# Kernel optimization log

Hardware: AMD Instinct MI355X
Metric: run time of the kernel (lower is better)

## Reference

```python
import jax, jax.numpy as jnp
import numpy as np

HEADS = 16
DIM_HEAD = 64
LN_EPS = 1e-3  # keras LayerNormalization default


def setup_inputs() -> dict:
    key = jax.random.key(0)
    ks = jax.random.split(key, 4)
    B, N, D = 8, 512, 1024
    inner = HEADS * DIM_HEAD  # 1024
    return {
        "x": jax.random.normal(ks[0], (B, N, D), dtype=jnp.float32),
        "w_qkv": jax.random.normal(ks[1], (D, 3 * inner), dtype=jnp.float32) * (D ** -0.5),
        "reattn_w": jax.random.normal(ks[2], (HEADS, HEADS), dtype=jnp.float32),
        "ln_gamma": jnp.ones((HEADS,), dtype=jnp.float32),
        "ln_beta": jnp.zeros((HEADS,), dtype=jnp.float32),
        "w_out": jax.random.normal(ks[3], (inner, D), dtype=jnp.float32) * (inner ** -0.5),
        "b_out": jnp.zeros((D,), dtype=jnp.float32),
    }


def reference(x, w_qkv, reattn_w, ln_gamma, ln_beta, w_out, b_out):
    B, N, D = x.shape
    H, dh = HEADS, DIM_HEAD
    scale = dh ** -0.5

    qkv = x @ w_qkv  # [B, N, 3*H*dh]
    q, k, v = jnp.split(qkv, 3, axis=-1)
    # b n (h d) -> b h n d
    to_heads = lambda t: t.reshape(B, N, H, dh).transpose(0, 2, 1, 3)
    q, k, v = to_heads(q), to_heads(k), to_heads(v)

    dots = jnp.einsum("bhid,bhjd->bhij", q, k) * scale  # [B, H, N, N]
    attn = jax.nn.softmax(dots, axis=-1)

    # re-attention: mix across heads
    attn = jnp.einsum("bhij,hg->bgij", attn, reattn_w)

    # LayerNorm over the head axis (axis=1), keras default eps
    mean = jnp.mean(attn, axis=1, keepdims=True)
    var = jnp.var(attn, axis=1, keepdims=True)
    attn = (attn - mean) * jax.lax.rsqrt(var + LN_EPS)
    attn = attn * ln_gamma[None, :, None, None] + ln_beta[None, :, None, None]

    out = jnp.einsum("bhij,bhjd->bhid", attn, v)  # [B, H, N, dh]
    out = out.transpose(0, 2, 1, 3).reshape(B, N, H * dh)  # b h n d -> b n (h d)
    return out @ w_out + b_out
```

## Files before the change

kernel.cpp:

```cpp
#include <hip/hip_runtime.h>
#include <math.h>

#define BB 8
#define NN 512
#define DD 1024
#define HH 16
#define DH 64
#define INNER 1024
#define QKV3 3072
#define PSTR (NN * NN + 64)

typedef __attribute__((ext_vector_type(8))) short short8;
typedef __attribute__((ext_vector_type(4))) float f32x4;

#define AS1 __attribute__((address_space(1)))
#define AS3 __attribute__((address_space(3)))

__device__ __forceinline__ float4 ld4(const float* p) { return *(const float4*)p; }

__device__ __forceinline__ unsigned short f2bf(float f) {
    unsigned u = __float_as_uint(f);
    return (unsigned short)((u + 0x7fffu + ((u >> 16) & 1u)) >> 16);
}
__device__ __forceinline__ float bf2f(unsigned short u) {
    return __uint_as_float(((unsigned)u) << 16);
}

__global__ void preprocess(const float* __restrict__ x, unsigned short* __restrict__ xb,
                           const float* __restrict__ wq, unsigned short* __restrict__ wqT,
                           const float* __restrict__ wo, unsigned short* __restrict__ woT) {
    __shared__ float t[32][33];
    const int tid = threadIdx.x;
    const int bx = blockIdx.x;
    if (bx < 4096) {
        size_t i = ((size_t)bx * 256 + tid) * 4;
        float4 v = ld4(x + i);
        ushort4 o;
        o.x = f2bf(v.x); o.y = f2bf(v.y); o.z = f2bf(v.z); o.w = f2bf(v.w);
        *(ushort4*)(xb + i) = o;
        return;
    }
    const float* in; unsigned short* out; int K, N, n0, k0;
    if (bx < 7168) {
        const int bb = bx - 4096;
        in = wq; out = wqT; K = DD; N = QKV3;
        n0 = (bb % 96) * 32; k0 = (bb / 96) * 32;
    } else {
        const int bb = bx - 7168;
        in = wo; out = woT; K = INNER; N = INNER;
        n0 = (bb & 31) * 32; k0 = (bb >> 5) * 32;
    }
    const int tx = tid & 31, ty = tid >> 5;
#pragma unroll
    for (int l = 0; l < 4; ++l)
        t[ty + 8 * l][tx] = in[(size_t)(k0 + ty + 8 * l) * N + n0 + tx];
    __syncthreads();
#pragma unroll
    for (int l = 0; l < 4; ++l)
        out[(size_t)(n0 + ty + 8 * l) * K + k0 + tx] = f2bf(t[tx][ty + 8 * l]);
}

__device__ __forceinline__ void stage128(const unsigned short* __restrict__ A,
                                         const unsigned short* __restrict__ Bt,
                                         int K, int bm, int bn, int kt,
                                         short* sb, int w, int l) {
#pragma unroll
    for (int t = 0; t < 2; ++t) {
        const int q = w * 2 + t;
        const int li = q * 512 + l * 8;
        const int row = li >> 5, kc = li & 31;
        __builtin_amdgcn_global_load_lds(
            (const AS1 void*)(A + (size_t)(bm + row) * K + kt * 32 + kc),
            (AS3 void*)(sb + q * 512), 16, 0, 0);
        __builtin_amdgcn_global_load_lds(
            (const AS1 void*)(Bt + (size_t)(bn + row) * K + kt * 32 + kc),
            (AS3 void*)(sb + 4096 + q * 512), 16, 0, 0);
    }
}

__global__ __launch_bounds__(256) void gemm_bf16(
    const unsigned short* __restrict__ A, const unsigned short* __restrict__ Bt,
    float* __restrict__ C, const float* __restrict__ bias, int M, int N, int K) {
    __shared__ __align__(16) short lds_[2 * 8192];
    const int tid = threadIdx.x;
    const int w = tid >> 6, l = tid & 63;
    const int bm = blockIdx.y * 128, bn = blockIdx.x * 128;
    const int wm = (w >> 1) * 64, wn = (w & 1) * 64;
    const int lrow = l & 15, lq = l >> 4;
    const int NT = K >> 5;

    f32x4 acc[4][4];
#pragma unroll
    for (int i = 0; i < 4; ++i)
#pragma unroll
        for (int j = 0; j < 4; ++j) acc[i][j] = (f32x4){0.f, 0.f, 0.f, 0.f};

    stage128(A, Bt, K, bm, bn, 0, lds_, w, l);
    asm volatile("s_waitcnt vmcnt(0)" ::: "memory");
    __builtin_amdgcn_s_barrier();

    for (int t = 0; t < NT; ++t) {
        const int s = t & 1;
        if (t + 1 < NT)
            stage128(A, Bt, K, bm, bn, t + 1, lds_ + (s ^ 1) * 8192, w, l);
        const short* As_ = lds_ + s * 8192;
        const short* Bs_ = As_ + 4096;
        short8 a[4], b[4];
#pragma unroll
        for (int i = 0; i < 4; ++i)
            a[i] = *(const short8*)(As_ + (wm + i * 16 + lrow) * 32 + lq * 8);
#pragma unroll
        for (int j = 0; j < 4; ++j)
            b[j] = *(const short8*)(Bs_ + (wn + j * 16 + lrow) * 32 + lq * 8);

        asm volatile("s_waitcnt lgkmcnt(0)" ::: "memory");
        __builtin_amdgcn_sched_barrier(0);

        __builtin_amdgcn_s_setprio(1);
#pragma unroll
        for (int i = 0; i < 4; ++i)
#pragma unroll
            for (int j = 0; j < 4; ++j)
                acc[i][j] = __builtin_amdgcn_mfma_f32_16x16x32_bf16(a[i], b[j], acc[i][j], 0, 0, 0);
        __builtin_amdgcn_s_setprio(0);

        asm volatile("s_waitcnt vmcnt(0)" ::: "memory");
        __builtin_amdgcn_s_barrier();
    }

#pragma unroll
    for (int i = 0; i < 4; ++i)
#pragma unroll
        for (int j = 0; j < 4; ++j) {
            const int col = bn + wn + j * 16 + lrow;
            const float bv = bias ? bias[col] : 0.f;
#pragma unroll
            for (int r = 0; r < 4; ++r) {
                const int row = bm + wm + i * 16 + lq * 4 + r;
                C[(size_t)row * N + col] = acc[i][j][r] + bv;
            }
        }
}

__device__ __forceinline__ void stage_st(const unsigned short* __restrict__ G, int K,
                                         int row0, int kt, short* dst_half,
                                         int w, int l) {
    const int grow = row0 + w * 16 + (l >> 2);
    const int gcol = kt * 32 + (((l & 3) * 8) ^ ((l & 32) ? 16 : 0));
    __builtin_amdgcn_global_load_lds(
        (const AS1 void*)(G + (size_t)grow * K + gcol),
        (AS3 void*)(dst_half + w * 512), 16, 0, 0);
}

__global__ __launch_bounds__(512, 4) void gemm256_bf(
    const unsigned short* __restrict__ A, const unsigned short* __restrict__ Bt,
    unsigned short* __restrict__ C, int M, int N, int K) {
    __shared__ __align__(16) short lds_[2 * 12288];
    const int tid = threadIdx.x;
    const int w = tid >> 6, l = tid & 63;
    const int wmi = w >> 1, wni = w & 1;
    const int lrow = l & 15, lq = l >> 4;
    const int bm = blockIdx.y * 256, bn = blockIdx.x * 128;
    const int NT = K >> 5;

    const int aoff = lrow * 32 + ((lq * 8) ^ ((lrow & 8) ? 16 : 0));

    f32x4 acc[4][4];
#pragma unroll
    for (int i = 0; i < 4; ++i)
#pragma unroll
        for (int j = 0; j < 4; ++j) acc[i][j] = (f32x4){0.f, 0.f, 0.f, 0.f};

    stage_st(A,  K, bm,       0, lds_ + 0,    w, l);
    stage_st(A,  K, bm + 128, 0, lds_ + 4096, w, l);
    stage_st(Bt, K, bn,       0, lds_ + 8192, w, l);
    asm volatile("s_waitcnt vmcnt(0)" ::: "memory");
    __builtin_amdgcn_s_barrier();

    for (int t = 0; t < NT; ++t) {
        const int s = t & 1;
        if (t + 1 < NT) {
            short* nb = lds_ + (s ^ 1) * 12288;
            stage_st(A,  K, bm,       t + 1, nb,        w, l);
            stage_st(A,  K, bm + 128, t + 1, nb + 4096, w, l);
            stage_st(Bt, K, bn,       t + 1, nb + 8192, w, l);
        }
        const short* cb = lds_ + s * 12288;
        short8 a[4], b[4];
#pragma unroll
        for (int i = 0; i < 4; ++i)
            a[i] = *(const short8*)(cb + (wmi * 4 + i) * 512 + aoff);
#pragma unroll
        for (int j = 0; j < 4; ++j)
            b[j] = *(const short8*)(cb + 8192 + (wni * 4 + j) * 512 + aoff);

        asm volatile("s_waitcnt lgkmcnt(0)" ::: "memory");
        __builtin_amdgcn_sched_barrier(0);

        __builtin_amdgcn_s_setprio(1);
#pragma unroll
        for (int i = 0; i < 4; ++i)
#pragma unroll
            for (int j = 0; j < 4; ++j)
                acc[i][j] = __builtin_amdgcn_mfma_f32_16x16x32_bf16(a[i], b[j], acc[i][j], 0, 0, 0);
        __builtin_amdgcn_s_setprio(0);

        asm volatile("s_waitcnt vmcnt(0)" ::: "memory");
        __builtin_amdgcn_s_barrier();
    }

#pragma unroll
    for (int i = 0; i < 4; ++i)
#pragma unroll
        for (int j = 0; j < 4; ++j) {
            const int col = bn + wni * 64 + j * 16 + lrow;
#pragma unroll
            for (int r = 0; r < 4; ++r) {
                const int row = bm + wmi * 64 + i * 16 + lq * 4 + r;
                C[(size_t)row * N + col] = f2bf(acc[i][j][r]);
            }
        }
}

__global__ __launch_bounds__(256) void scores_tv(
    const unsigned short* __restrict__ qkvb, unsigned short* __restrict__ attnb,
    unsigned short* __restrict__ vT, float* __restrict__ lsum2) {
    __shared__ unsigned short sh[256 * 64 + 4 * 16 * 68];
    const int bx = blockIdx.x;
    const int tid = threadIdx.x;

    if (bx >= 2048) {
        const int t = bx - 2048;
        const int j0 = (t & 15) * 32;
        const int d0 = ((t >> 4) & 1) * 32;
        const int bh = t >> 5;
        const int h = bh & 15, b = bh >> 4;
        unsigned short (*tt)[33] = (unsigned short(*)[33])sh;
        const int tx = tid & 31, ty = tid >> 5;
        const unsigned short* src = qkvb + (size_t)(b * NN) * QKV3 + 2 * INNER + h * DH;
#pragma unroll
        for (int k = 0; k < 4; ++k)
            tt[ty + 8 * k][tx] = src[(size_t)(j0 + ty + 8 * k) * QKV3 + d0 + tx];
        __syncthreads();
        unsigned short* dst = vT + (size_t)bh * DH * NN;
#pragma unroll
        for (int k = 0; k < 4; ++k)
            dst[(size_t)(d0 + ty + 8 * k) * NN + j0 + tx] = tt[tx][ty + 8 * k];
        return;
    }

    unsigned short* Ks = sh;
    unsigned short* obuf = sh + 16384;
    const int bh = bx & 127;
    const int h = bh & 15, b = bh >> 4;
    const int jh = (bx >> 7) & 1;
    const int w = tid >> 6, l = tid & 63;
    const int i0 = (bx >> 8) * 64 + w * 16;
    const int lrow = l & 15, lq = l >> 4;

    const unsigned short* kbase =
        qkvb + (size_t)(b * NN + jh * 256) * QKV3 + INNER + h * DH;
#pragma unroll
    for (int i = 0; i < 8; ++i) {
        const int r = (w * 8 + i) * 8 + (l >> 3);
        const int c = (l & 7) ^ (r & 7);
        __builtin_amdgcn_global_load_lds(
            (const AS1 void*)(kbase + (size_t)r * QKV3 + c * 8),
            (AS3 void*)(Ks + (w * 8 + i) * 512), 16, 0, 0);
    }

    const unsigned short* qb = qkvb + (size_t)(b * NN) * QKV3 + h * DH + lq * 8;
    const short8 qf0 = *(const short8*)(qb + (size_t)(i0 + lrow) * QKV3);
    const short8 qf1 = *(const short8*)(qb + (size_t)(i0 + lrow) * QKV3 + 32);

    asm volatile("s_waitcnt vmcnt(0)" ::: "memory");
    __syncthreads();

    unsigned short* obase = attnb + (size_t)bh * PSTR + (size_t)i0 * NN + jh * 256;
    unsigned short* ob = obuf + (w * 16) * 68;
    const int sw = lrow & 7;
    float lacc = 0.f;
#pragma unroll
    for (int jt = 0; jt < 16; ++jt) {
        const int R = jt * 16 + lrow;
        const short8 kf0 = *(const short8*)(Ks + R * 64 + ((lq ^ sw) * 8));
        const short8 kf1 = *(const short8*)(Ks + R * 64 + (((4 + lq) ^ sw) * 8));
        f32x4 acc = (f32x4){0.f, 0.f, 0.f, 0.f};
        acc = __builtin_amdgcn_mfma_f32_16x16x32_bf16(kf0, qf0, acc, 0, 0, 0);
        acc = __builtin_amdgcn_mfma_f32_16x16x32_bf16(kf1, qf1, acc, 0, 0, 0);
        float e0 = __expf(acc[0] * 0.125f);
        float e1 = __expf(acc[1] * 0.125f);
        float e2 = __expf(acc[2] * 0.125f);
        float e3 = __expf(acc[3] * 0.125f);
        lacc += (e0 + e1) + (e2 + e3);
        ushort4 o;
        o.x = f2bf(e0); o.y = f2bf(e1); o.z = f2bf(e2); o.w = f2bf(e3);
        *(ushort4*)(ob + lrow * 68 + (jt & 3) * 16 + lq * 4) = o;
        if ((jt & 3) == 3) {
            const int jb = (jt >> 2) * 64;
#pragma unroll
            for (int q = 0; q < 4; ++q) {
                const int rr = q * 4 + (l >> 4);
                const int cc = l & 15;
                *(ushort4*)(obase + (size_t)rr * NN + jb + cc * 4) =
                    *(const ushort4*)(ob + rr * 68 + cc * 4);
            }
        }
    }
    lacc += __shfl_xor(lacc, 16, 64);
    lacc += __shfl_xor(lacc, 32, 64);
    if (lq == 0)
        lsum2[(size_t)jh * BB * HH * NN + (size_t)bh * NN + i0 + lrow] = lacc;
}

__global__ void reattn_ln_bf(unsigned short* __restrict__ attnb,
                             const float* __restrict__ lsum2,
                             const float* __restrict__ rw,
                             const float* __restrict__ gamma,
                             const float* __restrict__ beta) {
    __shared__ float w[16][16];
    __shared__ float gs[16], bs[16];
    const int tid = threadIdx.x;
    ((float*)w)[tid] = rw[tid];
    if (tid < 16) { gs[tid] = gamma[tid]; bs[tid] = beta[tid]; }
    __syncthreads();

    const size_t idx = (size_t)blockIdx.x * 256 + tid;
    const int j4 = (int)(idx & 127);
    const int i = (int)((idx >> 7) & 511);
    const int b = (int)(idx >> 16);
    unsigned short* base = attnb + (size_t)(b * HH) * PSTR + (size_t)i * NN + j4 * 4;
    const float* l0 = lsum2 + (size_t)(b * HH) * NN + i;
    const float* l1 = l0 + (size_t)BB * HH * NN;

    float v[16][4];
#pragma unroll
    for (int h = 0; h < 16; ++h) {
        const float linv = 1.0f / (l0[h * NN] + l1[h * NN]);
        ushort4 u = *(const ushort4*)(base + (size_t)h * PSTR);
        v[h][0] = bf2f(u.x) * linv; v[h][1] = bf2f(u.y) * linv;
        v[h][2] = bf2f(u.z) * linv; v[h][3] = bf2f(u.w) * linv;
    }
    float o[16][4];
    float me[4] = {0.f, 0.f, 0.f, 0.f};
#pragma unroll
    for (int g = 0; g < 16; ++g) {
        float s0 = 0.f, s1 = 0.f, s2 = 0.f, s3 = 0.f;
#pragma unroll
        for (int h = 0; h < 16; ++h) {
            const float wg = w[h][g];
            s0 += v[h][0] * wg; s1 += v[h][1] * wg;
            s2 += v[h][2] * wg; s3 += v[h][3] * wg;
        }
        o[g][0] = s0; o[g][1] = s1; o[g][2] = s2; o[g][3] = s3;
        me[0] += s0; me[1] += s1; me[2] += s2; me[3] += s3;
    }
#pragma unroll
    for (int r = 0; r < 4; ++r) me[r] *= 0.0625f;
    float va[4] = {0.f, 0.f, 0.f, 0.f};
#pragma unroll
    for (int g = 0; g < 16; ++g)
#pragma unroll
        for (int r = 0; r < 4; ++r) {
            float d = o[g][r] - me[r];
            va[r] += d * d;
        }
    float ri[4];
#pragma unroll
    for (int r = 0; r < 4; ++r) ri[r] = rsqrtf(va[r] * 0.0625f + 1e-3f);
#pragma unroll
    for (int g = 0; g < 16; ++g) {
        ushort4 u;
        u.x = f2bf((o[g][0] - me[0]) * ri[0] * gs[g] + bs[g]);
        u.y = f2bf((o[g][1] - me[1]) * ri[1] * gs[g] + bs[g]);
        u.z = f2bf((o[g][2] - me[2]) * ri[2] * gs[g] + bs[g]);
        u.w = f2bf((o[g][3] - me[3]) * ri[3] * gs[g] + bs[g]);
        *(ushort4*)(base + (size_t)g * PSTR) = u;
    }
}

__device__ __forceinline__ void stage_pv(const unsigned short* __restrict__ pb,
                                         const unsigned short* __restrict__ vb,
                                         int j0, short* Ps, short* Vs,
                                         int w, int l, int lr8, int swd) {
#pragma unroll
    for (int t = 0; t < 4; ++t) {
        int c = w * 4 + t;
        int r = c * 8 + lr8;
        __builtin_amdgcn_global_load_lds(
            (const AS1 void*)(pb + (size_t)r * NN + j0 + swd),
            (AS3 void*)(Ps + c * 512), 16, 0, 0);
    }
#pragma unroll
    for (int t = 0; t < 2; ++t) {
        int c = w * 2 + t;
        int d = c * 8 + lr8;
        __builtin_amdgcn_global_load_lds(
            (const AS1 void*)(vb + (size_t)d * NN + j0 + swd),
            (AS3 void*)(Vs + c * 512), 16, 0, 0);
    }
}

__global__ __launch_bounds__(256) void pv_mfma(
    const unsigned short* __restrict__ attnb, const unsigned short* __restrict__ vT,
    unsigned short* __restrict__ outhb) {
    const int bh = blockIdx.x;
    const int h = bh & 15, b = bh >> 4;
    const int i0 = blockIdx.y * 128;
    __shared__ __align__(16) short Ps[2][128 * 64];
    __shared__ __align__(16) short Vs[2][64 * 64];
    const int tid = threadIdx.x;
    const int w = tid >> 6, l = tid & 63;
    const int lrow = l & 15, lq = l >> 4;
    const int lr8 = l >> 3;
    const int swd = ((l & 7) ^ (lr8 & 7)) * 8;

    f32x4 acc[2][4];
#pragma unroll
    for (int ic = 0; ic < 2; ++ic)
#pragma unroll
        for (int dt = 0; dt < 4; ++dt) acc[ic][dt] = (f32x4){0.f, 0.f, 0.f, 0.f};

    const unsigned short* pb = attnb + (size_t)bh * PSTR + (size_t)i0 * NN;
    const unsigned short* vb = vT + (size_t)bh * DH * NN;

    stage_pv(pb, vb, 0, Ps[0], Vs[0], w, l, lr8, swd);
    asm volatile("s_waitcnt vmcnt(0)" ::: "memory");
    __builtin_amdgcn_s_barrier();

    for (int js = 0; js < 8; ++js) {
        const int s = js & 1;
        if (js + 1 < 8)
            stage_pv(pb, vb, (js + 1) * 64, Ps[s ^ 1], Vs[s ^ 1], w, l, lr8, swd);

        short8 vf[8], pf[4];
#pragma unroll
        for (int kh = 0; kh < 2; ++kh) {
#pragma unroll
            for (int dt = 0; dt < 4; ++dt)
                vf[kh * 4 + dt] = *(const short8*)(
                    &Vs[s][(dt * 16 + lrow) * 64 + (((kh * 4 + lq) ^ (lrow & 7)) * 8)]);
#pragma unroll
            for (int ic = 0; ic < 2; ++ic)
                pf[kh * 2 + ic] = *(const short8*)(
                    &Ps[s][(w * 32 + ic * 16 + lrow) * 64 + (((kh * 4 + lq) ^ (lrow & 7)) * 8)]);
        }

        asm volatile("s_waitcnt lgkmcnt(0)" ::: "memory");
        __builtin_amdgcn_sched_barrier(0);

        __builtin_amdgcn_s_setprio(1);
#pragma unroll
        for (int kh = 0; kh < 2; ++kh)
#pragma unroll
            for (int ic = 0; ic < 2; ++ic)
#pragma unroll
                for (int dt = 0; dt < 4; ++dt)
                    acc[ic][dt] = __builtin_amdgcn_mfma_f32_16x16x32_bf16(
                        vf[kh * 4 + dt], pf[kh * 2 + ic], acc[ic][dt], 0, 0, 0);
        __builtin_amdgcn_s_setprio(0);

        asm volatile("s_waitcnt vmcnt(0)" ::: "memory");
        __builtin_amdgcn_s_barrier();
    }

#pragma unroll
    for (int ic = 0; ic < 2; ++ic) {
        unsigned short* orow = outhb +
            ((size_t)(b * NN + i0 + w * 32 + ic * 16 + lrow)) * INNER + h * DH + lq * 4;
#pragma unroll
        for (int dt = 0; dt < 4; ++dt) {
            ushort4 o;
            o.x = f2bf(acc[ic][dt][0]); o.y = f2bf(acc[ic][dt][1]);
            o.z = f2bf(acc[ic][dt][2]); o.w = f2bf(acc[ic][dt][3]);
            *(ushort4*)(orow + dt * 16) = o;
        }
    }
}

extern "C" void kernel_launch(void* const* d_in, const int* in_sizes, int n_in,
                              void* d_out, int out_size, void* d_ws, size_t ws_size,
                              hipStream_t stream) {
    const float* x        = (const float*)d_in[0];
    const float* w_qkv    = (const float*)d_in[1];
    const float* reattn_w = (const float*)d_in[2];
    const float* ln_gamma = (const float*)d_in[3];
    const float* ln_beta  = (const float*)d_in[4];
    const float* w_out    = (const float*)d_in[5];
    const float* b_out    = (const float*)d_in[6];
    float* out = (float*)d_out;

    unsigned short* qkvb  = (unsigned short*)d_ws;
    unsigned short* attnb = qkvb + (size_t)BB * NN * QKV3;
    unsigned short* vTb   = attnb + (size_t)BB * HH * PSTR;
    unsigned short* outhb = vTb + (size_t)BB * HH * DH * NN;
    unsigned short* xb    = outhb + (size_t)BB * NN * INNER;
    unsigned short* wqkvT = xb + (size_t)BB * NN * DD;
    unsigned short* woutT = wqkvT + (size_t)DD * QKV3;
    float*          lsum2 = (float*)(woutT + (size_t)INNER * INNER);

    dim3 blk(256);

    preprocess<<<dim3(8192), blk, 0, stream>>>(x, xb, w_qkv, wqkvT, w_out, woutT);

    gemm256_bf<<<dim3(QKV3 / 128, (BB * NN) / 256), dim3(512), 0, stream>>>(
        xb, wqkvT, qkvb, BB * NN, QKV3, DD);

    scores_tv<<<dim3(6144), blk, 0, stream>>>(qkvb, attnb, vTb, lsum2);

    reattn_ln_bf<<<dim3((BB * NN * NN) / 1024), blk, 0, stream>>>(
        attnb, lsum2, reattn_w, ln_gamma, ln_beta);

    pv_mfma<<<dim3(BB * HH, NN / 128), blk, 0, stream>>>(attnb, vTb, outhb);

    gemm_bf16<<<dim3(INNER / 128, (BB * NN) / 128), blk, 0, stream>>>(
        outhb, woutT, out, b_out, BB * NN, INNER, INNER);
}
```

Baseline: 201.9 us.

## Fuse re-attention LayerNorm into the PV matmul kernel

```diff
diff --git a/kernel.cpp b/kernel.cpp
--- a/kernel.cpp
+++ b/kernel.cpp
@@ -313,166 +313,129 @@
         lsum2[(size_t)jh * BB * HH * NN + (size_t)bh * NN + i0 + lrow] = lacc;
 }
 
-__global__ void reattn_ln_bf(unsigned short* __restrict__ attnb,
-                             const float* __restrict__ lsum2,
-                             const float* __restrict__ rw,
-                             const float* __restrict__ gamma,
-                             const float* __restrict__ beta) {
-    __shared__ float w[16][16];
-    __shared__ float gs[16], bs[16];
-    const int tid = threadIdx.x;
-    ((float*)w)[tid] = rw[tid];
-    if (tid < 16) { gs[tid] = gamma[tid]; bs[tid] = beta[tid]; }
-    __syncthreads();
-
-    const size_t idx = (size_t)blockIdx.x * 256 + tid;
-    const int j4 = (int)(idx & 127);
-    const int i = (int)((idx >> 7) & 511);
-    const int b = (int)(idx >> 16);
-    unsigned short* base = attnb + (size_t)(b * HH) * PSTR + (size_t)i * NN + j4 * 4;
-    const float* l0 = lsum2 + (size_t)(b * HH) * NN + i;
-    const float* l1 = l0 + (size_t)BB * HH * NN;
-
-    float v[16][4];
-#pragma unroll
-    for (int h = 0; h < 16; ++h) {
-        const float linv = 1.0f / (l0[h * NN] + l1[h * NN]);
-        ushort4 u = *(const ushort4*)(base + (size_t)h * PSTR);
-        v[h][0] = bf2f(u.x) * linv; v[h][1] = bf2f(u.y) * linv;
-        v[h][2] = bf2f(u.z) * linv; v[h][3] = bf2f(u.w) * linv;
-    }
-    float o[16][4];
-    float me[4] = {0.f, 0.f, 0.f, 0.f};
-#pragma unroll
-    for (int g = 0; g < 16; ++g) {
-        float s0 = 0.f, s1 = 0.f, s2 = 0.f, s3 = 0.f;
-#pragma unroll
-        for (int h = 0; h < 16; ++h) {
-            const float wg = w[h][g];
-            s0 += v[h][0] * wg; s1 += v[h][1] * wg;
-            s2 += v[h][2] * wg; s3 += v[h][3] * wg;
-        }
-        o[g][0] = s0; o[g][1] = s1; o[g][2] = s2; o[g][3] = s3;
-        me[0] += s0; me[1] += s1; me[2] += s2; me[3] += s3;
-    }
-#pragma unroll
-    for (int r = 0; r < 4; ++r) me[r] *= 0.0625f;
-    float va[4] = {0.f, 0.f, 0.f, 0.f};
-#pragma unroll
-    for (int g = 0; g < 16; ++g)
-#pragma unroll
-        for (int r = 0; r < 4; ++r) {
-            float d = o[g][r] - me[r];
-            va[r] += d * d;
-        }
-    float ri[4];
-#pragma unroll
-    for (int r = 0; r < 4; ++r) ri[r] = rsqrtf(va[r] * 0.0625f + 1e-3f);
-#pragma unroll
-    for (int g = 0; g < 16; ++g) {
-        ushort4 u;
-        u.x = f2bf((o[g][0] - me[0]) * ri[0] * gs[g] + bs[g]);
-        u.y = f2bf((o[g][1] - me[1]) * ri[1] * gs[g] + bs[g]);
-        u.z = f2bf((o[g][2] - me[2]) * ri[2] * gs[g] + bs[g]);
-        u.w = f2bf((o[g][3] - me[3]) * ri[3] * gs[g] + bs[g]);
-        *(ushort4*)(base + (size_t)g * PSTR) = u;
-    }
-}
-
-__device__ __forceinline__ void stage_pv(const unsigned short* __restrict__ pb,
-                                         const unsigned short* __restrict__ vb,
-                                         int j0, short* Ps, short* Vs,
-                                         int w, int l, int lr8, int swd) {
-#pragma unroll
-    for (int t = 0; t < 4; ++t) {
-        int c = w * 4 + t;
-        int r = c * 8 + lr8;
-        __builtin_amdgcn_global_load_lds(
-            (const AS1 void*)(pb + (size_t)r * NN + j0 + swd),
-            (AS3 void*)(Ps + c * 512), 16, 0, 0);
-    }
-#pragma unroll
-    for (int t = 0; t < 2; ++t) {
-        int c = w * 2 + t;
-        int d = c * 8 + lr8;
-        __builtin_amdgcn_global_load_lds(
-            (const AS1 void*)(vb + (size_t)d * NN + j0 + swd),
-            (AS3 void*)(Vs + c * 512), 16, 0, 0);
-    }
-}
-
-__global__ __launch_bounds__(256) void pv_mfma(
+__global__ __launch_bounds__(512) void reattn_pv(
     const unsigned short* __restrict__ attnb, const unsigned short* __restrict__ vT,
+    const float* __restrict__ lsum2, const float* __restrict__ rw,
+    const float* __restrict__ gamma, const float* __restrict__ beta,
     unsigned short* __restrict__ outhb) {
-    const int bh = blockIdx.x;
-    const int h = bh & 15, b = bh >> 4;
-    const int i0 = blockIdx.y * 128;
-    __shared__ __align__(16) short Ps[2][128 * 64];
-    __shared__ __align__(16) short Vs[2][64 * 64];
+    __shared__ unsigned short Ash[16 * 16 * 64];
+    __shared__ float wsh[16][16];
+    __shared__ float linv[16][16];
+    __shared__ float gsh[16], bsh[16];
+
+    const int b = blockIdx.x >> 5;
+    const int i0 = (blockIdx.x & 31) * 16;
     const int tid = threadIdx.x;
     const int w = tid >> 6, l = tid & 63;
     const int lrow = l & 15, lq = l >> 4;
-    const int lr8 = l >> 3;
-    const int swd = ((l & 7) ^ (lr8 & 7)) * 8;
+
+    if (tid < 256) {
+        ((float*)wsh)[tid] = rw[tid];
+        const int h = tid >> 4, i = tid & 15;
+        const float s =
+            lsum2[(size_t)(b * HH + h) * NN + i0 + i] +
+            lsum2[(size_t)BB * HH * NN + (size_t)(b * HH + h) * NN + i0 + i];
+        linv[h][i] = 1.0f / s;
+    }
+    if (tid < 16) { gsh[tid] = gamma[tid]; bsh[tid] = beta[tid]; }
+
+    const int ri = w * 2 + (l >> 5);
+    const int rj = (l & 31) * 2;
+    const unsigned short* ebase =
+        attnb + (size_t)(b * HH) * PSTR + (size_t)(i0 + ri) * NN + rj;
 
     f32x4 acc[2][4];
 #pragma unroll
-    for (int ic = 0; ic < 2; ++ic)
-#pragma unroll
-        for (int dt = 0; dt < 4; ++dt) acc[ic][dt] = (f32x4){0.f, 0.f, 0.f, 0.f};
-
-    const unsigned short* pb = attnb + (size_t)bh * PSTR + (size_t)i0 * NN;
-    const unsigned short* vb = vT + (size_t)bh * DH * NN;
-
-    stage_pv(pb, vb, 0, Ps[0], Vs[0], w, l, lr8, swd);
-    asm volatile("s_waitcnt vmcnt(0)" ::: "memory");
-    __builtin_amdgcn_s_barrier();
-
-    for (int js = 0; js < 8; ++js) {
-        const int s = js & 1;
-        if (js + 1 < 8)
-            stage_pv(pb, vb, (js + 1) * 64, Ps[s ^ 1], Vs[s ^ 1], w, l, lr8, swd);
-
-        short8 vf[8], pf[4];
-#pragma unroll
-        for (int kh = 0; kh < 2; ++kh) {
-#pragma unroll
-            for (int dt = 0; dt < 4; ++dt)
-                vf[kh * 4 + dt] = *(const short8*)(
-                    &Vs[s][(dt * 16 + lrow) * 64 + (((kh * 4 + lq) ^ (lrow & 7)) * 8)]);
-#pragma unroll
-            for (int ic = 0; ic < 2; ++ic)
-                pf[kh * 2 + ic] = *(const short8*)(
-                    &Ps[s][(w * 32 + ic * 16 + lrow) * 64 + (((kh * 4 + lq) ^ (lrow & 7)) * 8)]);
-        }
-
-        asm volatile("s_waitcnt lgkmcnt(0)" ::: "memory");
-        __builtin_amdgcn_sched_barrier(0);
-
-        __builtin_amdgcn_s_setprio(1);
-#pragma unroll
-        for (int kh = 0; kh < 2; ++kh)
-#pragma unroll
-            for (int ic = 0; ic < 2; ++ic)
-#pragma unroll
-                for (int dt = 0; dt < 4; ++dt)
-                    acc[ic][dt] = __builtin_amdgcn_mfma_f32_16x16x32_bf16(
-                        vf[kh * 4 + dt], pf[kh * 2 + ic], acc[ic][dt], 0, 0, 0);
-        __builtin_amdgcn_s_setprio(0);
-
-        asm volatile("s_waitcnt vmcnt(0)" ::: "memory");
-        __builtin_amdgcn_s_barrier();
-    }
-
-#pragma unroll
-    for (int ic = 0; ic < 2; ++ic) {
+    for (int gg = 0; gg < 2; ++gg)
+#pragma unroll
+        for (int dt = 0; dt < 4; ++dt) acc[gg][dt] = (f32x4){0.f, 0.f, 0.f, 0.f};
+
+    unsigned e[16];
+#pragma unroll
+    for (int h = 0; h < 16; ++h)
+        e[h] = *(const unsigned*)(ebase + (size_t)h * PSTR);
+
+    __syncthreads();
+
+    const int g0 = w * 2;
+    const int cch = rj >> 3;
+    const int csw = ((cch ^ (ri & 7)) << 3) + (rj & 7);
+
+    for (int jt = 0; jt < 8; ++jt) {
+        float e0[16], e1[16];
+#pragma unroll
+        for (int h = 0; h < 16; ++h) {
+            const float li = linv[h][ri];
+            e0[h] = bf2f((unsigned short)(e[h] & 0xffffu)) * li;
+            e1[h] = bf2f((unsigned short)(e[h] >> 16)) * li;
+        }
+        float m0[16], m1[16];
+        float mean0 = 0.f, mean1 = 0.f;
+#pragma unroll
+        for (int g = 0; g < 16; ++g) {
+            float s0 = 0.f, s1 = 0.f;
+#pragma unroll
+            for (int h = 0; h < 16; ++h) {
+                const float wg = wsh[h][g];
+                s0 += e0[h] * wg; s1 += e1[h] * wg;
+            }
+            m0[g] = s0; m1[g] = s1;
+            mean0 += s0; mean1 += s1;
+        }
+        mean0 *= 0.0625f; mean1 *= 0.0625f;
+        float va0 = 0.f, va1 = 0.f;
+#pragma unroll
+        for (int g = 0; g < 16; ++g) {
+            const float d0 = m0[g] - mean0, d1 = m1[g] - mean1;
+            va0 += d0 * d0; va1 += d1 * d1;
+        }
+        const float ri0 = rsqrtf(va0 * 0.0625f + 1e-3f);
+        const float ri1 = rsqrtf(va1 * 0.0625f + 1e-3f);
+#pragma unroll
+        for (int g = 0; g < 16; ++g) {
+            const unsigned short a0 = f2bf((m0[g] - mean0) * ri0 * gsh[g] + bsh[g]);
+            const unsigned short a1 = f2bf((m1[g] - mean1) * ri1 * gsh[g] + bsh[g]);
+            *(unsigned*)(&Ash[(g * 16 + ri) * 64 + csw]) = ((unsigned)a1 << 16) | (unsigned)a0;
+        }
+        __syncthreads();
+
+        if (jt < 7) {
+#pragma unroll
+            for (int h = 0; h < 16; ++h)
+                e[h] = *(const unsigned*)(ebase + (size_t)h * PSTR + (jt + 1) * 64);
+        }
+        const int j0 = jt * 64;
+#pragma unroll
+        for (int gg = 0; gg < 2; ++gg) {
+            const int g = g0 + gg;
+            const unsigned short* vb = vT + (size_t)(b * HH + g) * DH * NN;
+#pragma unroll
+            for (int kc = 0; kc < 2; ++kc) {
+                const int cc = kc * 4 + lq;
+                const short8 pf = *(const short8*)(
+                    &Ash[(g * 16 + lrow) * 64 + ((cc ^ (lrow & 7)) << 3)]);
+#pragma unroll
+                for (int dt = 0; dt < 4; ++dt) {
+                    const short8 vf = *(const short8*)(
+                        vb + (size_t)(dt * 16 + lrow) * NN + j0 + kc * 32 + lq * 8);
+                    acc[gg][dt] = __builtin_amdgcn_mfma_f32_16x16x32_bf16(
+                        vf, pf, acc[gg][dt], 0, 0, 0);
+                }
+            }
+        }
+        __syncthreads();
+    }
+
+#pragma unroll
+    for (int gg = 0; gg < 2; ++gg) {
+        const int g = g0 + gg;
         unsigned short* orow = outhb +
-            ((size_t)(b * NN + i0 + w * 32 + ic * 16 + lrow)) * INNER + h * DH + lq * 4;
+            (size_t)(b * NN + i0 + lrow) * INNER + g * DH + lq * 4;
 #pragma unroll
         for (int dt = 0; dt < 4; ++dt) {
             ushort4 o;
-            o.x = f2bf(acc[ic][dt][0]); o.y = f2bf(acc[ic][dt][1]);
-            o.z = f2bf(acc[ic][dt][2]); o.w = f2bf(acc[ic][dt][3]);
+            o.x = f2bf(acc[gg][dt][0]); o.y = f2bf(acc[gg][dt][1]);
+            o.z = f2bf(acc[gg][dt][2]); o.w = f2bf(acc[gg][dt][3]);
             *(ushort4*)(orow + dt * 16) = o;
         }
     }
@@ -508,10 +471,8 @@
 
     scores_tv<<<dim3(6144), blk, 0, stream>>>(qkvb, attnb, vTb, lsum2);
 
-    reattn_ln_bf<<<dim3((BB * NN * NN) / 1024), blk, 0, stream>>>(
-        attnb, lsum2, reattn_w, ln_gamma, ln_beta);
-
-    pv_mfma<<<dim3(BB * HH, NN / 128), blk, 0, stream>>>(attnb, vTb, outhb);
+    reattn_pv<<<dim3(BB * 32), dim3(512), 0, stream>>>(
+        attnb, vTb, lsum2, reattn_w, ln_gamma, ln_beta, outhb);
 
     gemm_bf16<<<dim3(INNER / 128, (BB * NN) / 128), blk, 0, stream>>>(
         outhb, woutT, out, b_out, BB * NN, INNER, INNER);
```

Measured after the change: 222.8 us. 10.4% more time.
